# Performance work log

Measured on AMD Instinct MI355X. Metric: run time of the kernel, lower is better.

## Reference

```python
import jax, jax.numpy as jnp
import numpy as np

PS = 4          # patch_size (square)
STRIDE = 2
PAD = (PS - 1) // 2
HEADS = 8
DIM = 256       # attn_dim == dim (kv_dim > dim, dim_reduc=1)
KV_DIM = 512
HD = DIM // HEADS
SCALE = HD ** -0.5
NP2 = PS * PS   # 16 elements per window


def _unfold(x, k, s, p):
    """torch.nn.functional.unfold: (B,C,H,W) -> (B, C*k*k, Ho*Wo)."""
    B, C, H, W = x.shape
    xp = jnp.pad(x, ((0, 0), (0, 0), (p, p), (p, p)))
    Ho = (H + 2 * p - k) // s + 1
    Wo = (W + 2 * p - k) // s + 1
    r = (jnp.arange(Ho) * s)[:, None] + jnp.arange(k)   # (Ho,k)
    c = (jnp.arange(Wo) * s)[:, None] + jnp.arange(k)   # (Wo,k)
    pt = xp[:, :, r][:, :, :, :, c]                     # (B,C,Ho,k,Wo,k)
    pt = pt.transpose(0, 1, 3, 5, 2, 4)                 # (B,C,k,k,Ho,Wo)
    return pt.reshape(B, C * k * k, Ho * Wo)


def _fold(y, C, Hout, Wout, k, s, p):
    """torch.nn.functional.fold: (B, C*k*k, Ho*Wo) -> (B,C,Hout,Wout), overlap-add."""
    B = y.shape[0]
    Ho = (Hout + 2 * p - k) // s + 1
    Wo = (Wout + 2 * p - k) // s + 1
    pt = y.reshape(B, C, k, k, Ho, Wo).transpose(0, 1, 4, 2, 5, 3)  # (B,C,Ho,k,Wo,k)
    r = (jnp.arange(Ho) * s)[:, None] + jnp.arange(k)
    c = (jnp.arange(Wo) * s)[:, None] + jnp.arange(k)
    out = jnp.zeros((B, C, Hout + 2 * p, Wout + 2 * p), y.dtype)
    out = out.at[:, :, r[:, :, None, None], c[None, None, :, :]].add(pt)
    return out[:, :, p:Hout + p, p:Wout + p]


def _patch_softmax(attn, Ht, Wt, Hb, Wb):
    """Normalize exp(attn) by per-bottom-pixel sums computed via a fold/unfold round trip
    (faithful to the original, including its reshape layout)."""
    a = jnp.exp(attn)                                                # (B*HtWt, H, 16, 1)
    s = a.reshape(-1, Ht * Wt, HEADS, NP2).transpose(0, 2, 3, 1)     # (B, H, 16, HtWt)
    s = s.reshape(-1, NP2, Ht * Wt)                                  # (B*H, 16, HtWt)
    s = _fold(s, 1, Hb, Wb, PS, STRIDE, PAD)                         # (B*H, 1, Hb, Wb)
    s = _unfold(s, PS, STRIDE, PAD).transpose(0, 2, 1)               # (B*H, HtWt, 16)
    s = jnp.where(s == 0, jnp.ones((), s.dtype), s)
    return a / s.reshape(-1, HEADS, NP2, 1)


def _forward(Xt, Xb, q_w, kv_w, proj_w, proj_b, rel_init, rel_bias, Ht, Wt, Hb, Wb):
    B, _, C = Xb.shape
    # im2col: gather 4x4 windows of the fine map, one window per coarse token
    Xbp = Xb.transpose(0, 2, 1).reshape(B, C, Hb, Wb)
    Xbp = _unfold(Xbp, PS, STRIDE, PAD)                              # (B, C*16, Ht*Wt)
    Xbp = Xbp.reshape(B, C, NP2, Ht * Wt).transpose(0, 3, 2, 1)
    Xbp = Xbp.reshape(B * Ht * Wt, NP2, C)                           # queries (top_down)
    Xtq = Xt.reshape(-1, 1, Xt.shape[-1])                            # (B*HtWt, 1, kv_dim)

    q = (Xbp @ q_w.T).reshape(-1, NP2, HEADS, HD).transpose(0, 2, 1, 3)  # (BHW,H,16,hd)
    kv = (Xtq @ kv_w.T).reshape(-1, 1, 2, HEADS, HD).transpose(2, 0, 3, 1, 4)
    k, v = kv[0], kv[1]                                              # (BHW,H,1,hd)

    attn = (q @ jnp.swapaxes(k, -2, -1)) * SCALE                     # (BHW,H,16,1)
    attn = attn + rel_init[:, None] + rel_bias[:, None]
    attn = _patch_softmax(attn, Ht, Wt, Hb, Wb)

    out = (attn @ v).transpose(0, 2, 1, 3).reshape(-1, NP2, DIM)     # (BHW,16,DIM)
    out = out.reshape(B, Ht * Wt, NP2, DIM).transpose(0, 3, 2, 1)
    out = out.reshape(B, DIM * NP2, Ht * Wt)
    out = _fold(out, DIM, Hb, Wb, PS, STRIDE, PAD)                   # (B,DIM,Hb,Wb)
    out = out.transpose(0, 2, 3, 1).reshape(B, Hb * Wb, DIM)
    return out @ proj_w.T + proj_b


def setup_inputs() -> dict:
    key = jax.random.key(0)
    ks = jax.random.split(key, 7)
    B, Ht, Wt, Hb, Wb = 4, 64, 64, 128, 128
    return {
        "Xt": jax.random.normal(ks[0], (B, Ht * Wt, KV_DIM), jnp.float32),
        "Xb": jax.random.normal(ks[1], (B, Hb * Wb, DIM), jnp.float32),
        "q_w": jax.random.normal(ks[2], (DIM, DIM), jnp.float32) * 0.02,
        "kv_w": jax.random.normal(ks[3], (2 * DIM, KV_DIM), jnp.float32) * 0.02,
        "proj_w": jax.random.normal(ks[4], (DIM, DIM), jnp.float32) * 0.02,
        "proj_b": jnp.zeros((DIM,), jnp.float32),
        "rel_init": jax.random.normal(ks[5], (NP2,), jnp.float32) * 0.02,
        "rel_bias": jax.random.normal(ks[6], (NP2,), jnp.float32) * 0.02,
        "Ht": Ht, "Wt": Wt, "Hb": Hb, "Wb": Wb,
    }


def reference(Xt, Xb, q_w, kv_w, proj_w, proj_b, rel_init, rel_bias, Ht, Wt, Hb, Wb):
    return _forward(Xt, Xb, q_w, kv_w, proj_w, proj_b, rel_init, rel_bias, Ht, Wt, Hb, Wb)
```

## Files before the change

kernel.cpp:

```cpp
#include <hip/hip_runtime.h>
#include <math.h>

constexpr int B_    = 4;
constexpr int HT    = 64,  WT = 64;
constexpr int HB    = 128, WB = 128;
constexpr int DIM   = 256;
constexpr int KVD   = 512;
constexpr int HEADS = 8;
constexpr int NP2   = 16;
constexpr int NPIX  = HB * WB;
constexpr int NWIN  = HT * WT;
constexpr float SCALE = 0.17677669529663687f;

using bf16x8 = __attribute__((ext_vector_type(8))) short;
using f32x4  = __attribute__((ext_vector_type(4))) float;

__device__ __forceinline__ unsigned short f2bf(float f) {
  union { float f; unsigned u; } v; v.f = f;
  unsigned r = v.u + 0x7fffu + ((v.u >> 16) & 1u);
  return (unsigned short)(r >> 16);
}
__device__ __forceinline__ unsigned pack_bf16(float x, float y) {
  unsigned ux = __float_as_uint(x) + 0x8000u;
  unsigned uy = __float_as_uint(y) + 0x8000u;
  return __builtin_amdgcn_perm(uy, ux, 0x07060302u);
}

constexpr int NXT4  = B_ * NWIN * KVD / 4;
constexpr int NQW4  = DIM * DIM / 4;
constexpr int NKVW4 = KVD * KVD / 4;
constexpr int NCAST4 = NXT4 + NQW4 + NKVW4 + NQW4;

__global__ __launch_bounds__(256) void cast_all(
    const float* __restrict__ Xt, const float* __restrict__ qw,
    const float* __restrict__ kvw, const float* __restrict__ pw,
    unsigned short* __restrict__ Xth, unsigned short* __restrict__ qwh,
    unsigned short* __restrict__ kvwh, unsigned short* __restrict__ pwh)
{
  const int i = blockIdx.x * 256 + threadIdx.x;
  const float* src; unsigned short* dst; int off;
  if (i < NXT4)                     { src = Xt;  dst = Xth;  off = i; }
  else if (i < NXT4 + NQW4)         { src = qw;  dst = qwh;  off = i - NXT4; }
  else if (i < NXT4 + NQW4 + NKVW4) { src = kvw; dst = kvwh; off = i - NXT4 - NQW4; }
  else                              { src = pw;  dst = pwh;  off = i - NXT4 - NQW4 - NKVW4; }
  float4 v = ((const float4*)src)[off];
  ushort4 o;
  o.x = f2bf(v.x); o.y = f2bf(v.y); o.z = f2bf(v.z); o.w = f2bf(v.w);
  ((ushort4*)dst)[off] = o;
}

template<bool AF32, int BN, bool BF16_OUT, bool BIAS>
__device__ __forceinline__ void gemm_core(
    const void* __restrict__ Ap, const unsigned short* __restrict__ Bw,
    const float* __restrict__ bias, void* __restrict__ Cp,
    int M, int N, int K, int bx, int by,
    unsigned short* Ash, unsigned short* Bsh)
{
  constexpr int NT = BN / 32;
  const int tid  = threadIdx.x;
  const int wave = tid >> 6;
  const int lane = tid & 63;
  const int m0 = bx * 128;
  const int n0 = by * BN;
  const int wm = (wave >> 1) * 64;
  const int wn = (wave & 1) * (BN / 2);

  f32x4 acc[4][NT];
#pragma unroll
  for (int i = 0; i < 4; ++i)
#pragma unroll
    for (int j = 0; j < NT; ++j) { f32x4 z = {0.f, 0.f, 0.f, 0.f}; acc[i][j] = z; }

  const float* Af = (const float*)Ap;
  float4 areg[4];
  auto loadA = [&](int kk) {
#pragma unroll
    for (int u = 0; u < 4; ++u) {
      const int c = u * 256 + tid, row = c >> 3, kq = (c & 7) * 4;
      areg[u] = *(const float4*)(Af + (size_t)(m0 + row) * K + kk + kq);
    }
  };
  if constexpr (AF32) loadA(0);

  const int fr = lane & 15;
  const int fk = (lane >> 4) * 8;

  for (int kk = 0; kk < K; kk += 32) {
    __syncthreads();
    if constexpr (AF32) {
#pragma unroll
      for (int u = 0; u < 4; ++u) {
        const int c = u * 256 + tid, row = c >> 3, kq = (c & 7) * 4;
        uint2 pk;
        pk.x = pack_bf16(areg[u].x, areg[u].y);
        pk.y = pack_bf16(areg[u].z, areg[u].w);
        *(uint2*)&Ash[row * 32 + kq] = pk;
      }
    } else {
      const unsigned short* Ab = (const unsigned short*)Ap;
#pragma unroll
      for (int i = 0; i < 2; ++i) {
        const int c = i * 256 + wave * 64 + lane, row = c >> 2, ko = (c & 3) * 8;
        __builtin_amdgcn_global_load_lds(
            (const __attribute__((address_space(1))) unsigned int*)
                (Ab + (size_t)(m0 + row) * K + kk + ko),
            (__attribute__((address_space(3))) unsigned int*)
                ((char*)Ash + i * 4096 + wave * 1024),
            16, 0, 0);
      }
    }
#pragma unroll
    for (int i = 0; i < BN / 64; ++i) {
      const int c = i * 256 + wave * 64 + lane, row = c >> 2, ko = (c & 3) * 8;
      __builtin_amdgcn_global_load_lds(
          (const __attribute__((address_space(1))) unsigned int*)
              (Bw + (size_t)(n0 + row) * K + kk + ko),
          (__attribute__((address_space(3))) unsigned int*)
              ((char*)Bsh + i * 4096 + wave * 1024),
          16, 0, 0);
    }
    __syncthreads();

    if constexpr (AF32) { if (kk + 32 < K) loadA(kk + 32); }

    bf16x8 af[4], bf[NT];
#pragma unroll
    for (int t = 0; t < 4; ++t)
      af[t] = *(const bf16x8*)&Ash[(wm + t * 16 + fr) * 32 + fk];
#pragma unroll
    for (int t = 0; t < NT; ++t)
      bf[t] = *(const bf16x8*)&Bsh[(wn + t * 16 + fr) * 32 + fk];
#pragma unroll
    for (int mt = 0; mt < 4; ++mt)
#pragma unroll
      for (int nt = 0; nt < NT; ++nt)
        acc[mt][nt] = __builtin_amdgcn_mfma_f32_16x16x32_bf16(
            af[mt], bf[nt], acc[mt][nt], 0, 0, 0);
  }

  const int col0 = lane & 15;
  const int rb   = (lane >> 4) * 4;
#pragma unroll
  for (int mt = 0; mt < 4; ++mt)
#pragma unroll
    for (int nt = 0; nt < NT; ++nt) {
      const int col = n0 + wn + nt * 16 + col0;
      float bv = BIAS ? bias[col] : 0.f;
#pragma unroll
      for (int r = 0; r < 4; ++r) {
        const int row = m0 + wm + mt * 16 + rb + r;
        const float v = acc[mt][nt][r] + bv;
        if (BF16_OUT) ((unsigned short*)Cp)[(size_t)row * N + col] = f2bf(v);
        else          ((float*)Cp)[(size_t)row * N + col] = v;
      }
    }
}

__global__ __launch_bounds__(256, 2) void g12_kernel(
    const float* __restrict__ Xb, const unsigned short* __restrict__ qwh,
    unsigned short* __restrict__ Qh,
    const unsigned short* __restrict__ Xth, const unsigned short* __restrict__ kvwh,
    unsigned short* __restrict__ KVh)
{
  __shared__ unsigned short Ash[128 * 32];
  __shared__ unsigned short Bsh[256 * 32];
  const int id = blockIdx.x;
  if ((id & 1) == 0) {
    gemm_core<true, 256, true, false>(Xb, qwh, nullptr, Qh,
        B_ * NPIX, DIM, DIM, id >> 1, 0, Ash, Bsh);
  } else {
    const int t = id >> 1;
    gemm_core<false, 128, true, false>(Xth, kvwh, nullptr, KVh,
        B_ * NWIN, KVD, KVD, t >> 2, t & 3, Ash, Bsh);
  }
}

__global__ __launch_bounds__(256, 2) void g3_kernel(
    const unsigned short* __restrict__ Oh, const unsigned short* __restrict__ pwh,
    const float* __restrict__ pb, float* __restrict__ out)
{
  __shared__ unsigned short Ash[128 * 32];
  __shared__ unsigned short Bsh[256 * 32];
  gemm_core<false, 256, false, true>(Oh, pwh, pb, out,
      B_ * NPIX, DIM, DIM, blockIdx.x, 0, Ash, Bsh);
}

__global__ __launch_bounds__(256) void es_kernel(
    const unsigned short* __restrict__ Qh, const unsigned short* __restrict__ KVh,
    const float* __restrict__ rel_init, const float* __restrict__ rel_bias,
    float* __restrict__ E, float* __restrict__ S)
{
  const int idx = blockIdx.x * 256 + threadIdx.x;
  const int h = idx & 7;
  const int x = (idx >> 3) & 127;
  const int y = (idx >> 10) & 127;
  const int b = idx >> 17;

  const uint4* qp = (const uint4*)(Qh + ((size_t)((b << 14) + y * WB + x)) * DIM + h * 32);
  uint4 q0 = qp[0], q1 = qp[1], q2 = qp[2], q3 = qp[3];
  const unsigned qa[16] = {q0.x,q0.y,q0.z,q0.w, q1.x,q1.y,q1.z,q1.w,
                           q2.x,q2.y,q2.z,q2.w, q3.x,q3.y,q3.z,q3.w};

  const int ilo = max(0, (y - 1) >> 1), ihi = min(HT - 1, (y + 1) >> 1);
  const int jlo = max(0, (x - 1) >> 1), jhi = min(WT - 1, (x + 1) >> 1);

  float s = 0.f;
  for (int i = ilo; i <= ihi; ++i)
    for (int j = jlo; j <= jhi; ++j) {
      const int w = i * WT + j;
      const int p = (y + 1 - 2 * i) * 4 + (x + 1 - 2 * j);
      const uint4* kp = (const uint4*)(KVh + ((size_t)((b << 12) + w)) * KVD + h * 32);
      uint4 k0 = kp[0], k1 = kp[1], k2 = kp[2], k3 = kp[3];
      const unsigned ka[16] = {k0.x,k0.y,k0.z,k0.w, k1.x,k1.y,k1.z,k1.w,
                               k2.x,k2.y,k2.z,k2.w, k3.x,k3.y,k3.z,k3.w};
      float acc = 0.f;
#pragma unroll
      for (int q = 0; q < 16; ++q) {
        acc = fmaf(__uint_as_float(qa[q] << 16),
                   __uint_as_float(ka[q] << 16), acc);
        acc = fmaf(__uint_as_float(qa[q] & 0xffff0000u),
                   __uint_as_float(ka[q] & 0xffff0000u), acc);
      }
      const float e = expf(acc * SCALE + rel_init[p] + rel_bias[p]);
      E[((size_t)((b << 12) + w)) * 128 + h * NP2 + p] = e;
      s += e;
    }
  S[(size_t)((b * HEADS + h) << 14) + y * WB + x] = s;
}

__global__ __launch_bounds__(256) void r_kernel(
    const float* __restrict__ E, const float* __restrict__ S,
    float* __restrict__ R)
{
  const int idx = blockIdx.x * 256 + threadIdx.x;
  const int b  = idx >> 19;
  const int r  = idx & 524287;
  const int w  = r >> 7;
  const int t7 = r & 127;
  const int h  = t7 >> 4, p = t7 & 15;

  const int h_eff = w >> 9;
  const int w_eff = ((w & 511) << 3) + h;
  const int i2 = w_eff >> 6, j2 = w_eff & 63;
  const int y2 = 2 * i2 + (p >> 2) - 1;
  const int x2 = 2 * j2 + (p & 3) - 1;
  float s = 1.f;
  if ((unsigned)y2 < (unsigned)HB && (unsigned)x2 < (unsigned)WB)
    s = S[(size_t)((b * HEADS + h_eff) * NPIX) + y2 * WB + x2];
  R[idx] = E[idx] / s;
}

__global__ __launch_bounds__(256) void o_kernel(
    const float* __restrict__ R, const unsigned short* __restrict__ KVh,
    unsigned short* __restrict__ out_pre)
{
  const int t  = threadIdx.x;
  const int pg = blockIdx.x * 8 + (t >> 5);
  const int b  = pg >> 14;
  const int yx = pg & 16383;
  const int y  = yx >> 7, x = yx & 127;
  const int c8 = t & 31;
  const int h  = c8 >> 2;

  const int ilo = max(0, (y - 1) >> 1), ihi = min(HT - 1, (y + 1) >> 1);
  const int jlo = max(0, (x - 1) >> 1), jhi = min(WT - 1, (x + 1) >> 1);

  float acc[8] = {};
  for (int i = ilo; i <= ihi; ++i)
    for (int j = jlo; j <= jhi; ++j) {
      const int w = i * WT + j;
      const int p = (y + 1 - 2 * i) * 4 + (x + 1 - 2 * j);
      const float rr = R[((size_t)(b * NWIN + w)) * 128 + h * NP2 + p];
      const uint4 v = *(const uint4*)(KVh + ((size_t)(b * NWIN + w)) * KVD + 256 + c8 * 8);
      const unsigned vv[4] = {v.x, v.y, v.z, v.w};
#pragma unroll
      for (int q = 0; q < 4; ++q) {
        acc[2*q]   = fmaf(rr, __uint_as_float(vv[q] << 16),         acc[2*q]);
        acc[2*q+1] = fmaf(rr, __uint_as_float(vv[q] & 0xffff0000u), acc[2*q+1]);
      }
    }

  uint4 ov;
  ov.x = (unsigned)f2bf(acc[0]) | ((unsigned)f2bf(acc[1]) << 16);
  ov.y = (unsigned)f2bf(acc[2]) | ((unsigned)f2bf(acc[3]) << 16);
  ov.z = (unsigned)f2bf(acc[4]) | ((unsigned)f2bf(acc[5]) << 16);
  ov.w = (unsigned)f2bf(acc[6]) | ((unsigned)f2bf(acc[7]) << 16);
  *(uint4*)(out_pre + (size_t)pg * DIM + c8 * 8) = ov;
}

extern "C" void kernel_launch(void* const* d_in, const int* in_sizes, int n_in,
                              void* d_out, int out_size, void* d_ws, size_t ws_size,
                              hipStream_t stream) {
  const float* Xt       = (const float*)d_in[0];
  const float* Xb       = (const float*)d_in[1];
  const float* q_w      = (const float*)d_in[2];
  const float* kv_w     = (const float*)d_in[3];
  const float* proj_w   = (const float*)d_in[4];
  const float* proj_b   = (const float*)d_in[5];
  const float* rel_init = (const float*)d_in[6];
  const float* rel_bias = (const float*)d_in[7];
  float* out = (float*)d_out;

  char* ws = (char*)d_ws;
  const size_t nXb = (size_t)B_ * NPIX * DIM;
  const size_t nXt = (size_t)B_ * NWIN * KVD;
  const size_t nQW = (size_t)DIM * DIM;
  const size_t nKVW = (size_t)KVD * KVD;
  unsigned short* Qh   = (unsigned short*)ws;  ws += nXb * 2;
  unsigned short* Xth  = (unsigned short*)ws;  ws += nXt * 2;
  unsigned short* KVh  = (unsigned short*)ws;  ws += nXt * 2;
  float*          E    = (float*)ws;           ws += (size_t)B_ * NWIN * 128 * 4;
  float*          S    = (float*)ws;           ws += (size_t)B_ * HEADS * NPIX * 4;
  unsigned short* qwh  = (unsigned short*)ws;  ws += nQW * 2;
  unsigned short* kvwh = (unsigned short*)ws;  ws += nKVW * 2;
  unsigned short* pwh  = (unsigned short*)ws;  ws += nQW * 2;
  float*          R    = (float*)Xth;
  unsigned short* Oh   = Qh;

  const dim3 blk(256);

  cast_all<<<dim3(NCAST4 / 256), blk, 0, stream>>>(
      Xt, q_w, kv_w, proj_w, Xth, qwh, kvwh, pwh);

  g12_kernel<<<dim3(1024), blk, 0, stream>>>(Xb, qwh, Qh, Xth, kvwh, KVh);

  es_kernel<<<dim3(B_ * NPIX * HEADS / 256), blk, 0, stream>>>(
      Qh, KVh, rel_init, rel_bias, E, S);

  r_kernel<<<dim3(B_ * NWIN * 128 / 256), blk, 0, stream>>>(E, S, R);

  o_kernel<<<dim3(B_ * NPIX / 8), blk, 0, stream>>>(R, KVh, Oh);

  g3_kernel<<<dim3(B_ * NPIX / 128), blk, 0, stream>>>(Oh, pwh, proj_b, out);
}
```

Before: 253.2 us.

## Software-pipeline GEMM core with multi-buffered LDS and explicit vmcnt waits

Restructures the shared GEMM core so global-to-LDS loads for the next K-step(s) are issued before computing the current one. The bf16-A path uses triple buffering and the fp32-A path double buffering, with manual s_waitcnt and s_barrier instead of two __syncthreads per step. This hides global memory latency behind MFMA work, at the cost of larger LDS footprints that may limit occupancy, and relies on hand-counted vmcnt values.

```diff
diff --git a/kernel.cpp b/kernel.cpp
--- a/kernel.cpp
+++ b/kernel.cpp
@@ -26,6 +26,11 @@
   return __builtin_amdgcn_perm(uy, ux, 0x07060302u);
 }
 
+__device__ __forceinline__ void wait_vm0() { asm volatile("s_waitcnt vmcnt(0)" ::: "memory"); }
+__device__ __forceinline__ void wait_vm4() { asm volatile("s_waitcnt vmcnt(4)" ::: "memory"); }
+__device__ __forceinline__ void wait_vm6() { asm volatile("s_waitcnt vmcnt(6)" ::: "memory"); }
+__device__ __forceinline__ void wait_lgkm0() { asm volatile("s_waitcnt lgkmcnt(0)" ::: "memory"); }
+
 constexpr int NXT4  = B_ * NWIN * KVD / 4;
 constexpr int NQW4  = DIM * DIM / 4;
 constexpr int NKVW4 = KVD * KVD / 4;
@@ -57,6 +62,7 @@
     unsigned short* Ash, unsigned short* Bsh)
 {
   constexpr int NT = BN / 32;
+  constexpr int NB = BN / 64;
   const int tid  = threadIdx.x;
   const int wave = tid >> 6;
   const int lane = tid & 63;
@@ -71,32 +77,89 @@
 #pragma unroll
     for (int j = 0; j < NT; ++j) { f32x4 z = {0.f, 0.f, 0.f, 0.f}; acc[i][j] = z; }
 
-  const float* Af = (const float*)Ap;
-  float4 areg[4];
-  auto loadA = [&](int kk) {
-#pragma unroll
-    for (int u = 0; u < 4; ++u) {
-      const int c = u * 256 + tid, row = c >> 3, kq = (c & 7) * 4;
-      areg[u] = *(const float4*)(Af + (size_t)(m0 + row) * K + kk + kq);
-    }
-  };
-  if constexpr (AF32) loadA(0);
-
   const int fr = lane & 15;
   const int fk = (lane >> 4) * 8;
-
-  for (int kk = 0; kk < K; kk += 32) {
-    __syncthreads();
-    if constexpr (AF32) {
+  const int niter = K >> 5;
+
+  auto stageB = [&](int kk, int buf) {
+#pragma unroll
+    for (int i = 0; i < NB; ++i) {
+      const int c = i * 256 + wave * 64 + lane, row = c >> 2, ko = (c & 3) * 8;
+      __builtin_amdgcn_global_load_lds(
+          (const __attribute__((address_space(1))) unsigned int*)
+              (Bw + (size_t)(n0 + row) * K + kk + ko),
+          (__attribute__((address_space(3))) unsigned int*)
+              ((char*)Bsh + buf * (BN * 64) + i * 4096 + wave * 1024),
+          16, 0, 0);
+    }
+  };
+
+  auto compute = [&](int bufA, int bufB) {
+    bf16x8 af[4], bfr[NT];
+    const unsigned short* Abase = Ash + bufA * 4096;
+    const unsigned short* Bbase = Bsh + bufB * (BN * 32);
+#pragma unroll
+    for (int x = 0; x < 4; ++x)
+      af[x] = *(const bf16x8*)&Abase[(wm + x * 16 + fr) * 32 + fk];
+#pragma unroll
+    for (int x = 0; x < NT; ++x)
+      bfr[x] = *(const bf16x8*)&Bbase[(wn + x * 16 + fr) * 32 + fk];
+#pragma unroll
+    for (int mt = 0; mt < 4; ++mt)
+#pragma unroll
+      for (int nt = 0; nt < NT; ++nt)
+        acc[mt][nt] = __builtin_amdgcn_mfma_f32_16x16x32_bf16(
+            af[mt], bfr[nt], acc[mt][nt], 0, 0, 0);
+  };
+
+  if constexpr (AF32) {
+    const float* Af = (const float*)Ap;
+    float4 areg[4];
+    auto loadA = [&](int kk) {
+#pragma unroll
+      for (int u = 0; u < 4; ++u) {
+        const int c = u * 256 + tid, row = c >> 3, kq = (c & 7) * 4;
+        areg[u] = *(const float4*)(Af + (size_t)(m0 + row) * K + kk + kq);
+      }
+    };
+    auto writeA = [&](int buf) {
 #pragma unroll
       for (int u = 0; u < 4; ++u) {
         const int c = u * 256 + tid, row = c >> 3, kq = (c & 7) * 4;
         uint2 pk;
         pk.x = pack_bf16(areg[u].x, areg[u].y);
         pk.y = pack_bf16(areg[u].z, areg[u].w);
-        *(uint2*)&Ash[row * 32 + kq] = pk;
-      }
-    } else {
+        *(uint2*)&Ash[buf * 4096 + row * 32 + kq] = pk;
+      }
+    };
+
+    loadA(0);
+    stageB(0, 0);
+    writeA(0);
+    loadA(32);
+    wait_vm4();
+    wait_lgkm0();
+    __builtin_amdgcn_s_barrier();
+
+    for (int t = 0; t < niter; ++t) {
+      const int cur = t & 1;
+      const int kk = t << 5;
+      if (t + 1 < niter) stageB(kk + 32, cur ^ 1);
+      compute(cur, cur);
+      if (t + 1 < niter) {
+        writeA(cur ^ 1);
+        if (t + 2 < niter) {
+          loadA(kk + 64);
+          wait_vm4();
+        } else {
+          wait_vm0();
+        }
+        wait_lgkm0();
+        __builtin_amdgcn_s_barrier();
+      }
+    }
+  } else {
+    auto stageA = [&](int kk, int buf) {
       const unsigned short* Ab = (const unsigned short*)Ap;
 #pragma unroll
       for (int i = 0; i < 2; ++i) {
@@ -105,37 +168,32 @@
             (const __attribute__((address_space(1))) unsigned int*)
                 (Ab + (size_t)(m0 + row) * K + kk + ko),
             (__attribute__((address_space(3))) unsigned int*)
-                ((char*)Ash + i * 4096 + wave * 1024),
+                ((char*)Ash + buf * 8192 + i * 4096 + wave * 1024),
             16, 0, 0);
       }
-    }
-#pragma unroll
-    for (int i = 0; i < BN / 64; ++i) {
-      const int c = i * 256 + wave * 64 + lane, row = c >> 2, ko = (c & 3) * 8;
-      __builtin_amdgcn_global_load_lds(
-          (const __attribute__((address_space(1))) unsigned int*)
-              (Bw + (size_t)(n0 + row) * K + kk + ko),
-          (__attribute__((address_space(3))) unsigned int*)
-              ((char*)Bsh + i * 4096 + wave * 1024),
-          16, 0, 0);
-    }
-    __syncthreads();
-
-    if constexpr (AF32) { if (kk + 32 < K) loadA(kk + 32); }
-
-    bf16x8 af[4], bf[NT];
-#pragma unroll
-    for (int t = 0; t < 4; ++t)
-      af[t] = *(const bf16x8*)&Ash[(wm + t * 16 + fr) * 32 + fk];
-#pragma unroll
-    for (int t = 0; t < NT; ++t)
-      bf[t] = *(const bf16x8*)&Bsh[(wn + t * 16 + fr) * 32 + fk];
-#pragma unroll
-    for (int mt = 0; mt < 4; ++mt)
-#pragma unroll
-      for (int nt = 0; nt < NT; ++nt)
-        acc[mt][nt] = __builtin_amdgcn_mfma_f32_16x16x32_bf16(
-            af[mt], bf[nt], acc[mt][nt], 0, 0, 0);
+    };
+    auto wait_batch = [&]() {
+      if constexpr (NB == 2) wait_vm4(); else wait_vm6();
+    };
+
+    stageA(0, 0);  stageB(0, 0);
+    stageA(32, 1); stageB(32, 1);
+    wait_batch();
+    __builtin_amdgcn_s_barrier();
+
+    int rd = 0, wr = 2;
+    for (int t = 0; t < niter; ++t) {
+      const int kk = t << 5;
+      if (t + 2 < niter) { stageA(kk + 64, wr); stageB(kk + 64, wr); }
+      compute(rd, rd);
+      if (t + 1 < niter) {
+        if (t + 2 < niter) wait_batch();
+        else               wait_vm0();
+        __builtin_amdgcn_s_barrier();
+      }
+      rd = (rd == 2) ? 0 : rd + 1;
+      wr = (wr == 2) ? 0 : wr + 1;
+    }
   }
 
   const int col0 = lane & 15;
@@ -162,8 +220,8 @@
     const unsigned short* __restrict__ Xth, const unsigned short* __restrict__ kvwh,
     unsigned short* __restrict__ KVh)
 {
-  __shared__ unsigned short Ash[128 * 32];
-  __shared__ unsigned short Bsh[256 * 32];
+  __shared__ unsigned short Ash[3 * 128 * 32];
+  __shared__ unsigned short Bsh[2 * 256 * 32];
   const int id = blockIdx.x;
   if ((id & 1) == 0) {
     gemm_core<true, 256, true, false>(Xb, qwh, nullptr, Qh,
@@ -179,8 +237,8 @@
     const unsigned short* __restrict__ Oh, const unsigned short* __restrict__ pwh,
     const float* __restrict__ pb, float* __restrict__ out)
 {
-  __shared__ unsigned short Ash[128 * 32];
-  __shared__ unsigned short Bsh[256 * 32];
+  __shared__ unsigned short Ash[3 * 128 * 32];
+  __shared__ unsigned short Bsh[3 * 256 * 32];
   gemm_core<false, 256, false, true>(Oh, pwh, pb, out,
       B_ * NPIX, DIM, DIM, blockIdx.x, 0, Ash, Bsh);
 }
```

Result: no change. 258.1 us (+1.9%).
